# Kernel tuning notes

Measured on AMD Instinct MI355X. Metric: run time of the kernel, lower is better.

Reference implementation:

```python
import jax, jax.numpy as jnp
import numpy as np
import math

FREQ_DIM = 161
OUTPUT_DIM = 4096
RNN_DIM = 128
EMBED_DIM = 32


def conv2d(x, w, b, stride):
    # x: (B, Cin, H, W), w: (Cout, Cin, kh, kw)
    out = jax.lax.conv_general_dilated(x, w, window_strides=stride, padding='VALID',
                                       dimension_numbers=('NCHW', 'OIHW', 'NCHW'))
    return out + b[None, :, None, None]


def gru_seq(x, w_ih, w_hh, b_ih, b_hh, h0):
    # x: (B, T, D); PyTorch GRU gate order: r, z, n
    B, T, D = x.shape
    H = h0.shape[-1]
    xg = jnp.einsum('btd,gd->btg', x, w_ih) + b_ih  # (B, T, 3H)

    def step(h, xg_t):
        hg = h @ w_hh.T + b_hh
        xr, xz, xn = jnp.split(xg_t, 3, axis=-1)
        hr, hz, hn = jnp.split(hg, 3, axis=-1)
        r = jax.nn.sigmoid(xr + hr)
        z = jax.nn.sigmoid(xz + hz)
        n = jnp.tanh(xn + r * hn)
        h_new = (1 - z) * n + z * h
        return h_new, h_new

    _, hs = jax.lax.scan(step, h0, jnp.swapaxes(xg, 0, 1))
    return jnp.swapaxes(hs, 0, 1)  # (B, T, H)


def gru_cell(ix, h, w_ih, w_hh, b_ih, b_hh):
    xg = ix @ w_ih.T + b_ih
    hg = h @ w_hh.T + b_hh
    xr, xz, xn = jnp.split(xg, 3, axis=-1)
    hr, hz, hn = jnp.split(hg, 3, axis=-1)
    r = jax.nn.sigmoid(xr + hr)
    z = jax.nn.sigmoid(xz + hz)
    n = jnp.tanh(xn + r * hn)
    return (1 - z) * n + z * h


def attend(eh, dhx):
    # eh: (B, T, H), dhx: (B, H)
    scores = jnp.einsum('bth,bh->bt', eh, dhx)
    a = jax.nn.softmax(scores, axis=-1)
    return jnp.einsum('bth,bt->bh', eh, a)


def setup_inputs() -> dict:
    key = jax.random.key(0)
    ks = jax.random.split(key, 16)

    def rn(k, shape, fan_in):
        s = 1.0 / math.sqrt(fan_in)
        return jax.random.uniform(k, shape, jnp.float32, -s, s)

    B, T_audio, L = 32, 512, 128
    x = jax.random.normal(ks[0], (B, T_audio, FREQ_DIM), jnp.float32)
    y = jax.random.randint(ks[1], (B, L), 0, OUTPUT_DIM)

    conv_in = 544  # 17 * 32 after two convs on freq dim 161
    params = {
        'conv1_w': rn(ks[2], (32, 1, 5, 32), 1 * 5 * 32),
        'conv1_b': rn(ks[3], (32,), 1 * 5 * 32),
        'conv2_w': rn(ks[4], (32, 32, 5, 32), 32 * 5 * 32),
        'conv2_b': rn(ks[5], (32,), 32 * 5 * 32),
        'rnn_w_ih': rn(ks[6], (3 * RNN_DIM, conv_in), RNN_DIM),
        'rnn_w_hh': rn(ks[7], (3 * RNN_DIM, RNN_DIM), RNN_DIM),
        'rnn_b_ih': rn(ks[8], (3 * RNN_DIM,), RNN_DIM),
        'rnn_b_hh': rn(ks[9], (3 * RNN_DIM,), RNN_DIM),
        'emb': jax.random.normal(ks[10], (OUTPUT_DIM, EMBED_DIM), jnp.float32),
        'dec_w_ih': rn(ks[11], (3 * RNN_DIM, EMBED_DIM), RNN_DIM),
        'dec_w_hh': rn(ks[12], (3 * RNN_DIM, RNN_DIM), RNN_DIM),
        'dec_b_ih': rn(ks[13], (3 * RNN_DIM,), RNN_DIM),
        'dec_b_hh': rn(ks[14], (3 * RNN_DIM,), RNN_DIM),
        'fc_w': rn(ks[15], (OUTPUT_DIM, RNN_DIM), RNN_DIM),
        'fc_b': rn(jax.random.fold_in(key, 99), (OUTPUT_DIM,), RNN_DIM),
        'h_init': jnp.zeros((1, RNN_DIM), jnp.float32),
    }
    return {'x': x, 'y': y, **params}


def forward(x, y, conv1_w, conv1_b, conv2_w, conv2_b,
            rnn_w_ih, rnn_w_hh, rnn_b_ih, rnn_b_hh,
            emb, dec_w_ih, dec_w_hh, dec_b_ih, dec_b_hh,
            fc_w, fc_b, h_init):
    B = x.shape[0]
    h = x[:, None, :, :]  # (B, 1, T, F)
    h = jax.nn.relu(conv2d(h, conv1_w, conv1_b, (2, 2)))
    h = jax.nn.relu(conv2d(h, conv2_w, conv2_b, (2, 2)))  # (B, 32, t, f)
    h = jnp.transpose(h, (0, 2, 3, 1))  # (B, t, f, c)
    b, t, f, c = h.shape
    h = h.reshape(b, t, f * c)
    eh = gru_seq(h, rnn_w_ih, rnn_w_hh, rnn_b_ih, rnn_b_hh,
                 jnp.zeros((b, RNN_DIM), h.dtype))  # (B, t, 128)

    inputs = emb[y[:, :-1]]  # (B, L-1, 32)
    hx = jnp.broadcast_to(h_init, (B, RNN_DIM))
    hx = hx + attend(eh, hx)

    def step(hx, ix):
        hx = gru_cell(ix, hx, dec_w_ih, dec_w_hh, dec_b_ih, dec_b_hh)
        hx = hx + attend(eh, hx)
        return hx, hx

    _, outs = jax.lax.scan(step, hx, jnp.swapaxes(inputs, 0, 1))
    out = jnp.concatenate([hx[:, None, :], jnp.swapaxes(outs, 0, 1)], axis=1)  # (B, L, 128)
    logits = jnp.einsum('btd,od->bto', out, fc_w) + fc_b
    return logits


def reference(x, y, conv1_w, conv1_b, conv2_w, conv2_b,
              rnn_w_ih, rnn_w_hh, rnn_b_ih, rnn_b_hh,
              emb, dec_w_ih, dec_w_hh, dec_b_ih, dec_b_hh,
              fc_w, fc_b, h_init):
    return forward(x, y, conv1_w, conv1_b, conv2_w, conv2_b,
                   rnn_w_ih, rnn_w_hh, rnn_b_ih, rnn_b_hh,
                   emb, dec_w_ih, dec_w_hh, dec_b_ih, dec_b_hh,
                   fc_w, fc_b, h_init)
```

## Files before the change

kernel.cpp:

```cpp
#include <hip/hip_runtime.h>
#include <stdint.h>

typedef unsigned short u16;
typedef uint32_t u32;

typedef __bf16 bf16x8 __attribute__((ext_vector_type(8)));
typedef float f32x4 __attribute__((ext_vector_type(4)));
typedef _Float16 h2v __attribute__((ext_vector_type(2)));

union B8 { uint4 q; u32 u[4]; bf16x8 v; };

__device__ __forceinline__ u16 f2bf(float f) {
  u32 u = __float_as_uint(f);
  u32 r = (u + 0x7fffu + ((u >> 16) & 1u)) >> 16;
  return (u16)r;
}
__device__ __forceinline__ u16 f2h(float f) {
  union { _Float16 h; u16 u; } v; v.h = (_Float16)f; return v.u;
}
__device__ __forceinline__ float dot2h(u32 a, u32 b, float c) {
  union U { u32 u; h2v v; } A, B; A.u = a; B.u = b;
  return __builtin_amdgcn_fdot2(A.v, B.v, c, false);
}
__device__ __forceinline__ float sigf(float x) { return 1.f / (1.f + __expf(-x)); }
__device__ __forceinline__ float tanhf_fast(float x) {
  x = fminf(fmaxf(x, -15.f), 15.f);
  float e = __expf(2.f * x);
  return (e - 1.f) / (e + 1.f);
}

__global__ __launch_bounds__(256) void prep_k(
    const float* rnn_w_hh, const float* dec_w_hh, const float* conv1_w,
    const float* conv2_w, const float* rnn_w_ih, const float* dec_w_ih,
    const float* fc_w, const float* emb, const int* y,
    u32* wT2e, u32* wT2d, u16* w1b, u16* w2b, u16* wihb, u16* dwihb,
    u16* fcwb, u16* adec)
{
  int e = blockIdx.x * 256 + threadIdx.x;
  const int S0 = 24576, S1 = 24576, S2 = 5120, S3 = 163840, S4 = 208896,
            S5 = 12288, S6 = 524288, S7 = 130048;
  if (e < S0) { int g = e >> 6, k2 = e & 63;
    wT2e[e] = (u32)f2h(rnn_w_hh[g*128 + 2*k2]) | ((u32)f2h(rnn_w_hh[g*128 + 2*k2 + 1]) << 16);
    return; }
  e -= S0;
  if (e < S1) { int g = e >> 6, k2 = e & 63;
    wT2d[e] = (u32)f2h(dec_w_hh[g*128 + 2*k2]) | ((u32)f2h(dec_w_hh[g*128 + 2*k2 + 1]) << 16);
    return; }
  e -= S1;
  if (e < S2) { int kh = e >> 10, c = (e >> 5) & 31, kw = e & 31;
    w1b[e] = f2bf(conv1_w[c*160 + kh*32 + kw]); return; }
  e -= S2;
  if (e < S3) { int kt = e >> 10, c = (e >> 5) & 31, kw = e & 31;
    int ic = kt / 5, kh = kt - ic * 5;
    w2b[e] = f2bf(conv2_w[((c*32 + ic)*5 + kh)*32 + kw]); return; }
  e -= S3;
  if (e < S4) { wihb[e] = f2bf(rnn_w_ih[e]); return; }
  e -= S4;
  if (e < S5) { dwihb[e] = f2bf(dec_w_ih[e]); return; }
  e -= S5;
  if (e < S6) { fcwb[e] = f2bf(fc_w[e]); return; }
  e -= S6;
  if (e < S7) { int m = e >> 5, k = e & 31;
    int b = m / 127, t = m - b * 127;
    adec[e] = f2bf(emb[y[b*128 + t]*32 + k]); return; }
}

__global__ __launch_bounds__(256) void conv1_k(const float* x, const u16* w1b,
                                               const float* c1b, u16* in1b)
{
  __shared__ __align__(16) u16 slab[35 * 162];
  __shared__ __align__(16) u16 wl[5120];
  int b = blockIdx.x >> 4;
  int oh0 = (blockIdx.x & 15) * 16;
  int ih0 = oh0 * 2;
  for (int e = threadIdx.x; e < 35 * 161; e += 256) {
    int r = e / 161, iw = e - r * 161;
    int ih = ih0 + r;
    float v = (ih < 512) ? x[(b*512 + ih)*161 + iw] : 0.f;
    slab[r*162 + iw] = f2bf(v);
  }
  for (int e = threadIdx.x; e < 5120; e += 256) wl[e] = w1b[e];
  __syncthreads();
  int lane = threadIdx.x & 63, wid = threadIdx.x >> 6;
  int lrow = lane & 15, lk = (lane >> 4) * 8;
  B8 bw[5][2];
  #pragma unroll
  for (int kt = 0; kt < 5; kt++)
    #pragma unroll
    for (int ct = 0; ct < 2; ct++)
      bw[kt][ct].q = *(const uint4*)&wl[(kt*32 + ct*16 + lrow)*32 + lk];
  float bias0 = c1b[lrow], bias1 = c1b[16 + lrow];
  for (int mt = wid; mt < 65; mt += 4) {
    int m = mt * 16 + lrow;
    int ohl = m / 65, ow = m - ohl * 65;
    int ro = ohl * 324 + ow * 2 + lk;
    f32x4 a0, a1;
    #pragma unroll
    for (int i = 0; i < 4; i++) { a0[i] = 0.f; a1[i] = 0.f; }
    #pragma unroll
    for (int kt = 0; kt < 5; kt++) {
      B8 af;
      const u32* p = (const u32*)&slab[ro + kt * 162];
      af.u[0] = p[0]; af.u[1] = p[1]; af.u[2] = p[2]; af.u[3] = p[3];
      a0 = __builtin_amdgcn_mfma_f32_16x16x32_bf16(af.v, bw[kt][0].v, a0, 0, 0, 0);
      a1 = __builtin_amdgcn_mfma_f32_16x16x32_bf16(af.v, bw[kt][1].v, a1, 0, 0, 0);
    }
    int rb = mt * 16 + (lane >> 4) * 4;
    #pragma unroll
    for (int i = 0; i < 4; i++) {
      int mr = rb + i;
      int ohl2 = mr / 65, ow2 = mr - ohl2 * 65;
      int oh = oh0 + ohl2;
      if (oh < 254) {
        float v0 = fmaxf(a0[i] + bias0, 0.f);
        float v1 = fmaxf(a1[i] + bias1, 0.f);
        in1b[((b*32 + lrow)*254 + oh)*72 + ow2] = f2bf(v0);
        in1b[((b*32 + 16 + lrow)*254 + oh)*72 + ow2] = f2bf(v1);
      }
    }
  }
}

__global__ __launch_bounds__(256) void conv2_k(const u16* in1b, const u16* w2b,
                                               const float* c2b, u16* hbf)
{
  extern __shared__ char smem[];
  u16* slab = (u16*)smem;
  u16* wl = (u16*)(smem + 87552);
  int b = blockIdx.x >> 4;
  int oh0 = (blockIdx.x & 15) * 8;
  int ih0 = oh0 * 2;
  for (int q = threadIdx.x; q < 5472; q += 256) {
    int ic = q / 171;
    int rem = q - ic * 171;
    int r = rem / 9, j = rem - r * 9;
    int ih = ih0 + r;
    uint4 v = make_uint4(0u, 0u, 0u, 0u);
    if (ih < 254) v = *(const uint4*)&in1b[(((b*32 + ic)*254 + ih)*72) + j*8];
    *(uint4*)&slab[(ic*19 + r)*72 + j*8] = v;
  }
  int lane = threadIdx.x & 63, wid = threadIdx.x >> 6;
  int lrow = lane & 15, lk = (lane >> 4) * 8;
  int ohl_[3], ow_[3];
  #pragma unroll
  for (int q = 0; q < 3; q++) {
    int mt = (q == 2) ? 8 : (wid + q * 4);
    int m = mt * 16 + lrow;
    if (m > 135) m = 0;
    ohl_[q] = m / 17; ow_[q] = m - ohl_[q] * 17;
  }
  f32x4 acc[3][2];
  #pragma unroll
  for (int q = 0; q < 3; q++)
    #pragma unroll
    for (int ct = 0; ct < 2; ct++)
      #pragma unroll
      for (int i = 0; i < 4; i++) acc[q][ct][i] = 0.f;

  for (int ph = 0; ph < 5; ph++) {
    __syncthreads();
    {
      const uint4* s4 = (const uint4*)&w2b[ph * 32768];
      uint4* d4 = (uint4*)wl;
      for (int q = threadIdx.x; q < 4096; q += 256) d4[q] = s4[q];
    }
    __syncthreads();
    for (int ktl = 0; ktl < 32; ktl++) {
      int ktg = ph * 32 + ktl;
      int ic = ktg / 5, kh = ktg - ic * 5;
      B8 fb0, fb1;
      fb0.q = *(const uint4*)&wl[(ktl*32 + lrow)*32 + lk];
      fb1.q = *(const uint4*)&wl[(ktl*32 + 16 + lrow)*32 + lk];
      int base = (ic * 19 + kh) * 72 + lk;
      #pragma unroll
      for (int q = 0; q < 3; q++) {
        if (q == 2 && wid != 0) break;
        B8 af;
        const u32* p = (const u32*)&slab[base + ohl_[q] * 144 + ow_[q] * 2];
        af.u[0] = p[0]; af.u[1] = p[1]; af.u[2] = p[2]; af.u[3] = p[3];
        acc[q][0] = __builtin_amdgcn_mfma_f32_16x16x32_bf16(af.v, fb0.v, acc[q][0], 0, 0, 0);
        acc[q][1] = __builtin_amdgcn_mfma_f32_16x16x32_bf16(af.v, fb1.v, acc[q][1], 0, 0, 0);
      }
    }
  }
  #pragma unroll
  for (int q = 0; q < 3; q++) {
    if (q == 2 && wid != 0) break;
    int mt = (q == 2) ? 8 : (wid + q * 4);
    int rb = mt * 16 + (lane >> 4) * 4;
    #pragma unroll
    for (int ct = 0; ct < 2; ct++) {
      int c = ct * 16 + lrow;
      float bias = c2b[c];
      #pragma unroll
      for (int i = 0; i < 4; i++) {
        int mr = rb + i;
        if (mr < 136) {
          int ohl = mr / 17, ow = mr - ohl * 17;
          int oh = oh0 + ohl;
          if (oh < 125) {
            float v = fmaxf(acc[q][ct][i] + bias, 0.f);
            hbf[(b*125 + oh)*544 + ow*32 + c] = f2bf(v);
          }
        }
      }
    }
  }
}

__global__ __launch_bounds__(256) void gemm_k(const u16* A, const u16* Bw,
                                              const float* bias, float* C,
                                              int M, int N, int K)
{
  __shared__ __align__(16) u16 As[64 * 32];
  __shared__ __align__(16) u16 Bs[64 * 32];
  int m0 = blockIdx.x * 64, n0 = blockIdx.y * 64;
  int tid = threadIdx.x;
  int lane = tid & 63, wid = tid >> 6;
  int lrow = lane & 15, lk = (lane >> 4) * 8;
  int sr = tid >> 2, sc8 = (tid & 3) * 8;
  f32x4 acc[4];
  #pragma unroll
  for (int nt = 0; nt < 4; nt++)
    #pragma unroll
    for (int i = 0; i < 4; i++) acc[nt][i] = 0.f;
  int nkt = K >> 5;
  for (int kt = 0; kt < nkt; kt++) {
    __syncthreads();
    uint4 va = make_uint4(0u, 0u, 0u, 0u);
    int arow = m0 + sr;
    if (arow < M) va = *(const uint4*)&A[arow * K + kt * 32 + sc8];
    *(uint4*)&As[sr * 32 + sc8] = va;
    uint4 vb = *(const uint4*)&Bw[(n0 + sr) * K + kt * 32 + sc8];
    *(uint4*)&Bs[sr * 32 + sc8] = vb;
    __syncthreads();
    B8 af; af.q = *(const uint4*)&As[(wid * 16 + lrow) * 32 + lk];
    #pragma unroll
    for (int nt = 0; nt < 4; nt++) {
      B8 bb; bb.q = *(const uint4*)&Bs[(nt * 16 + lrow) * 32 + lk];
      acc[nt] = __builtin_amdgcn_mfma_f32_16x16x32_bf16(af.v, bb.v, acc[nt], 0, 0, 0);
    }
  }
  #pragma unroll
  for (int nt = 0; nt < 4; nt++) {
    int col = n0 + nt * 16 + lrow;
    float bv = bias[col];
    #pragma unroll
    for (int i = 0; i < 4; i++) {
      int row = m0 + wid * 16 + (lane >> 4) * 4 + i;
      if (row < M) C[row * N + col] = acc[nt][i] + bv;
    }
  }
}

__global__ __launch_bounds__(1024, 1) void enc_k(const u32* wT2, const float* xg,
                                                 const float* bhh_g, u16* ehk, u16* eht)
{
  __shared__ __align__(16) u32 hp[2][2][64];
  __shared__ float hg[2][1152];
  int tid = threadIdx.x;
  int g = tid >> 9, tb = tid & 511, kh = tb >> 7, t = tb & 127;
  int b = blockIdx.x * 2 + g;
  u32 w0[16], w1[16], w2[16];
  {
    const uint4* p0 = (const uint4*)(wT2 + (size_t)t * 64 + kh * 16);
    const uint4* p1 = (const uint4*)(wT2 + (size_t)(128 + t) * 64 + kh * 16);
    const uint4* p2 = (const uint4*)(wT2 + (size_t)(256 + t) * 64 + kh * 16);
    #pragma unroll
    for (int j = 0; j < 4; j++) {
      uint4 q0 = p0[j]; w0[4*j] = q0.x; w0[4*j+1] = q0.y; w0[4*j+2] = q0.z; w0[4*j+3] = q0.w;
      uint4 q1 = p1[j]; w1[4*j] = q1.x; w1[4*j+1] = q1.y; w1[4*j+2] = q1.z; w1[4*j+3] = q1.w;
      uint4 q2 = p2[j]; w2[4*j] = q2.x; w2[4*j+1] = q2.y; w2[4*j+2] = q2.z; w2[4*j+3] = q2.w;
    }
  }
  float b0 = 0.f, b1 = 0.f, b2 = 0.f, xr0 = 0.f, xr1 = 0.f, xr2 = 0.f, hreg = 0.f;
  if (kh == 0) {
    b0 = bhh_g[t]; b1 = bhh_g[128 + t]; b2 = bhh_g[256 + t];
    const float* xp = &xg[(size_t)b * 125 * 384];
    xr0 = xp[t]; xr1 = xp[128 + t]; xr2 = xp[256 + t];
    ((u16*)&hp[g][0][0])[t] = 0;
  }
  __syncthreads();
  for (int tt = 0; tt < 125; tt++) {
    const u32* hb = &hp[g][tt & 1][kh * 16];
    float r0 = 0.f, r1 = 0.f, z0 = 0.f, z1 = 0.f, n0 = 0.f, n1 = 0.f;
    #pragma unroll
    for (int j = 0; j < 4; j++) {
      uint4 hv = *(const uint4*)&hb[4*j];
      r0 = dot2h(w0[4*j+0], hv.x, r0); r1 = dot2h(w0[4*j+1], hv.y, r1);
      r0 = dot2h(w0[4*j+2], hv.z, r0); r1 = dot2h(w0[4*j+3], hv.w, r1);
      z0 = dot2h(w1[4*j+0], hv.x, z0); z1 = dot2h(w1[4*j+1], hv.y, z1);
      z0 = dot2h(w1[4*j+2], hv.z, z0); z1 = dot2h(w1[4*j+3], hv.w, z1);
      n0 = dot2h(w2[4*j+0], hv.x, n0); n1 = dot2h(w2[4*j+1], hv.y, n1);
      n0 = dot2h(w2[4*j+2], hv.z, n0); n1 = dot2h(w2[4*j+3], hv.w, n1);
    }
    if (kh) {
      float* hh = &hg[g][(kh - 1) * 384];
      hh[t] = r0 + r1; hh[128 + t] = z0 + z1; hh[256 + t] = n0 + n1;
    }
    __syncthreads();
    if (kh == 0) {
      const float* hh = &hg[g][0];
      float pr = r0 + r1 + hh[t] + hh[384 + t] + hh[768 + t];
      float pz = z0 + z1 + hh[128 + t] + hh[512 + t] + hh[896 + t];
      float pn = n0 + n1 + hh[256 + t] + hh[640 + t] + hh[1024 + t];
      float r = sigf(xr0 + pr + b0);
      float z = sigf(xr1 + pz + b1);
      float n = tanhf_fast(xr2 + r * (pn + b2));
      hreg = (1.f - z) * n + z * hreg;
      u16 hv = f2h(hreg);
      ((u16*)&hp[g][(tt & 1) ^ 1][0])[t] = hv;
      ehk[((size_t)(b*64 + (t >> 1)) * 125 + tt) * 2 + (t & 1)] = hv;
      eht[((size_t)(b*128 + t)) * 128 + tt] = hv;
      if (tt + 1 < 125) {
        const float* xq = &xg[((size_t)b * 125 + tt + 1) * 384];
        xr0 = xq[t]; xr1 = xq[128 + t]; xr2 = xq[256 + t];
      }
    }
    __syncthreads();
  }
  if (kh == 0) {
    size_t rb = ((size_t)(b*128 + t)) * 128;
    eht[rb + 125] = 0; eht[rb + 126] = 0; eht[rb + 127] = 0;
  }
}

__global__ __launch_bounds__(1024, 1) void dec_k(const u32* wT2, const u32* ehk_g,
                                                 const u32* eht_g, const float* xgd,
                                                 const float* bhh_g, const float* h_init,
                                                 u16* outb)
{
  extern __shared__ char sm[];
  int tid = threadIdx.x;
  int g = tid >> 9, tb = tid & 511, kh = tb >> 7, t = tb & 127;
  int b = blockIdx.x * 2 + g;
  char* base = sm + (size_t)g * 41024;
  u32* elK   = (u32*)base;
  float* hgP = (float*)(base + 32000);
  float* sp  = (float*)(base + 36608);
  float* ctxB= (float*)(base + 38656);
  u16* hxA   = (u16*)(base + 40192);
  u16* hxB   = (u16*)(base + 40448);
  u16* scp   = (u16*)(base + 40704);
  float* red = (float*)(base + 40960);

  u32 w0[16], w1[16], w2[16];
  {
    const uint4* p0 = (const uint4*)(wT2 + (size_t)t * 64 + kh * 16);
    const uint4* p1 = (const uint4*)(wT2 + (size_t)(128 + t) * 64 + kh * 16);
    const uint4* p2 = (const uint4*)(wT2 + (size_t)(256 + t) * 64 + kh * 16);
    #pragma unroll
    for (int j = 0; j < 4; j++) {
      uint4 q0 = p0[j]; w0[4*j] = q0.x; w0[4*j+1] = q0.y; w0[4*j+2] = q0.z; w0[4*j+3] = q0.w;
      uint4 q1 = p1[j]; w1[4*j] = q1.x; w1[4*j+1] = q1.y; w1[4*j+2] = q1.z; w1[4*j+3] = q1.w;
      uint4 q2 = p2[j]; w2[4*j] = q2.x; w2[4*j+1] = q2.y; w2[4*j+2] = q2.z; w2[4*j+3] = q2.w;
    }
  }
  u32 rowr[16];
  {
    const uint4* rp = (const uint4*)(eht_g + (size_t)b * 8192 + (size_t)t * 64 + kh * 16);
    #pragma unroll
    for (int j = 0; j < 4; j++) {
      uint4 q = rp[j]; rowr[4*j] = q.x; rowr[4*j+1] = q.y; rowr[4*j+2] = q.z; rowr[4*j+3] = q.w;
    }
  }
  for (int e = tb; e < 8000; e += 512) elK[e] = ehk_g[(size_t)b * 8000 + e];
  float b0 = 0.f, b1 = 0.f, b2 = 0.f, xr0 = 0.f, xr1 = 0.f, xr2 = 0.f;
  float hxf = 0.f, hxg = 0.f;
  if (kh == 0) {
    b0 = bhh_g[t]; b1 = bhh_g[128 + t]; b2 = bhh_g[256 + t];
    hxf = h_init[t];
    const float* xp = &xgd[(size_t)b * 127 * 384];
    xr0 = xp[t]; xr1 = xp[128 + t]; xr2 = xp[256 + t];
  }
  __syncthreads();

  for (int step = 0; step < 128; step++) {
    if (step > 0) {
      const u32* hb = (const u32*)hxB + kh * 16;
      float r0 = 0.f, r1 = 0.f, z0 = 0.f, z1 = 0.f, n0 = 0.f, n1 = 0.f;
      #pragma unroll
      for (int j = 0; j < 4; j++) {
        uint4 hv = *(const uint4*)&hb[4*j];
        r0 = dot2h(w0[4*j+0], hv.x, r0); r1 = dot2h(w0[4*j+1], hv.y, r1);
        r0 = dot2h(w0[4*j+2], hv.z, r0); r1 = dot2h(w0[4*j+3], hv.w, r1);
        z0 = dot2h(w1[4*j+0], hv.x, z0); z1 = dot2h(w1[4*j+1], hv.y, z1);
        z0 = dot2h(w1[4*j+2], hv.z, z0); z1 = dot2h(w1[4*j+3], hv.w, z1);
        n0 = dot2h(w2[4*j+0], hv.x, n0); n1 = dot2h(w2[4*j+1], hv.y, n1);
        n0 = dot2h(w2[4*j+2], hv.z, n0); n1 = dot2h(w2[4*j+3], hv.w, n1);
      }
      if (kh) {
        float* hh = &hgP[(kh - 1) * 384];
        hh[t] = r0 + r1; hh[128 + t] = z0 + z1; hh[256 + t] = n0 + n1;
      }
      __syncthreads();
      if (kh == 0) {
        float pr = r0 + r1 + hgP[t] + hgP[384 + t] + hgP[768 + t];
        float pz = z0 + z1 + hgP[128 + t] + hgP[512 + t] + hgP[896 + t];
        float pn = n0 + n1 + hgP[256 + t] + hgP[640 + t] + hgP[1024 + t];
        float r = sigf(xr0 + pr + b0);
        float z = sigf(xr1 + pz + b1);
        float n = tanhf_fast(xr2 + r * (pn + b2));
        hxg = (1.f - z) * n + z * hxf;
        ((u16*)hxA)[t] = f2h(hxg);
        if (step < 127) {
          const float* xq = &xgd[((size_t)b * 127 + step) * 384];
          xr0 = xq[t]; xr1 = xq[128 + t]; xr2 = xq[256 + t];
        }
      }
      __syncthreads();
    } else {
      if (kh == 0) { hxg = hxf; ((u16*)hxA)[t] = f2h(hxg); }
      __syncthreads();
    }
    {
      float s0 = 0.f, s1 = 0.f;
      const u32* ek = &elK[(kh * 16) * 125];
      const u32* hxA4 = (const u32*)hxA;
      #pragma unroll
      for (int j = 0; j < 4; j++) {
        uint4 aw = *(const uint4*)&hxA4[kh * 16 + 4*j];
        s0 = dot2h(ek[(4*j+0)*125 + t], aw.x, s0);
        s1 = dot2h(ek[(4*j+1)*125 + t], aw.y, s1);
        s0 = dot2h(ek[(4*j+2)*125 + t], aw.z, s0);
        s1 = dot2h(ek[(4*j+3)*125 + t], aw.w, s1);
      }
      sp[kh * 128 + t] = s0 + s1;
    }
    __syncthreads();
    if (kh == 0) {
      float s = (t < 125) ? (sp[t] + sp[128 + t] + sp[256 + t] + sp[384 + t]) : -1e30f;
      float mw = s;
      #pragma unroll
      for (int o = 32; o > 0; o >>= 1) mw = fmaxf(mw, __shfl_xor(mw, o));
      float ev = (t < 125) ? __expf(s - mw) : 0.f;
      float sw = ev;
      #pragma unroll
      for (int o = 32; o > 0; o >>= 1) sw += __shfl_xor(sw, o);
      ((u16*)scp)[t] = f2h(ev);
      if ((t & 63) == 0) { int wv = t >> 6; red[wv*2] = mw; red[wv*2 + 1] = sw; }
    }
    __syncthreads();
    float m0r = red[0], S0r = red[1], m1r = red[2], S1r = red[3];
    float M = fmaxf(m0r, m1r);
    float f0 = __expf(m0r - M), f1 = __expf(m1r - M);
    float inv = 1.f / (f0 * S0r + f1 * S1r);
    float c0 = 0.f, c1 = 0.f;
    {
      const u32* scp4 = (const u32*)scp;
      #pragma unroll
      for (int j = 0; j < 4; j++) {
        uint4 sw4 = *(const uint4*)&scp4[kh * 16 + 4*j];
        c0 = dot2h(rowr[4*j+0], sw4.x, c0); c1 = dot2h(rowr[4*j+1], sw4.y, c1);
        c0 = dot2h(rowr[4*j+2], sw4.z, c0); c1 = dot2h(rowr[4*j+3], sw4.w, c1);
      }
    }
    if (kh) ctxB[(kh - 1) * 128 + t] = c0 + c1;
    __syncthreads();
    if (kh == 0) {
      float ctx = ((c0 + c1) + ctxB[t]) * f0 + (ctxB[128 + t] + ctxB[256 + t]) * f1;
      hxf = hxg + ctx * inv;
      outb[((size_t)(b * 128) + step) * 128 + t] = f2bf(hxf);
      ((u16*)hxB)[t] = f2h(hxf);
    }
    __syncthreads();
  }
}

extern "C" void kernel_launch(void* const* d_in, const int* in_sizes, int n_in,
                              void* d_out, int out_size, void* d_ws, size_t ws_size,
                              hipStream_t stream)
{
  const float* x        = (const float*)d_in[0];
  const int*   y        = (const int*)d_in[1];
  const float* conv1_w  = (const float*)d_in[2];
  const float* conv1_b  = (const float*)d_in[3];
  const float* conv2_w  = (const float*)d_in[4];
  const float* conv2_b  = (const float*)d_in[5];
  const float* rnn_w_ih = (const float*)d_in[6];
  const float* rnn_w_hh = (const float*)d_in[7];
  const float* rnn_b_ih = (const float*)d_in[8];
  const float* rnn_b_hh = (const float*)d_in[9];
  const float* emb      = (const float*)d_in[10];
  const float* dec_w_ih = (const float*)d_in[11];
  const float* dec_w_hh = (const float*)d_in[12];
  const float* dec_b_ih = (const float*)d_in[13];
  const float* dec_b_hh = (const float*)d_in[14];
  const float* fc_w     = (const float*)d_in[15];
  const float* fc_b     = (const float*)d_in[16];
  const float* h_init   = (const float*)d_in[17];
  float* logits = (float*)d_out;

  char* ws = (char*)d_ws;
  size_t off = 0;
  auto alloc = [&](size_t bytes) { char* p = ws + off; off = (off + bytes + 255) & ~(size_t)255; return p; };
  u16* in1b  = (u16*)alloc(37453824);
  u16* hbf   = (u16*)alloc(4352000);
  float* xge = (float*)alloc(6144000);
  u32* ehb_k = (u32*)alloc(1024000);
  u32* ehb_t = (u32*)alloc(1048576);
  float* xgd = (float*)alloc(6242304);
  u16* adec  = (u16*)alloc(260096);
  u16* outb  = (u16*)alloc(1048576);
  u32* wT2e  = (u32*)alloc(98304);
  u32* wT2d  = (u32*)alloc(98304);
  u16* w1b   = (u16*)alloc(10240);
  u16* w2b   = (u16*)alloc(327680);
  u16* wihb  = (u16*)alloc(417792);
  u16* dwihb = (u16*)alloc(24576);
  u16* fcwb  = (u16*)alloc(1048576);

  hipFuncSetAttribute((const void*)conv2_k, hipFuncAttributeMaxDynamicSharedMemorySize, 153088);
  hipFuncSetAttribute((const void*)dec_k,   hipFuncAttributeMaxDynamicSharedMemorySize, 82048);

  prep_k<<<4272, 256, 0, stream>>>(rnn_w_hh, dec_w_hh, conv1_w, conv2_w, rnn_w_ih,
                                   dec_w_ih, fc_w, emb, y,
                                   wT2e, wT2d, w1b, w2b, wihb, dwihb, fcwb, adec);
  conv1_k<<<512, 256, 0, stream>>>(x, w1b, conv1_b, in1b);
  conv2_k<<<512, 256, 153088, stream>>>(in1b, w2b, conv2_b, hbf);
  gemm_k<<<dim3(63, 6), 256, 0, stream>>>(hbf, wihb, rnn_b_ih, xge, 4000, 384, 544);
  gemm_k<<<dim3(64, 6), 256, 0, stream>>>(adec, dwihb, dec_b_ih, xgd, 4064, 384, 32);
  enc_k<<<16, 1024, 0, stream>>>(wT2e, xge, rnn_b_hh, (u16*)ehb_k, (u16*)ehb_t);
  dec_k<<<16, 1024, 82048, stream>>>(wT2d, ehb_k, ehb_t, xgd, dec_b_hh, h_init, outb);
  gemm_k<<<dim3(64, 64), 256, 0, stream>>>(outb, fcwb, fc_b, logits, 4096, 4096, 128);
}
```

Before: 604.0 us.

## Reduce K-split partials with wave shuffles instead of LDS and barriers

Remaps threads so the four K-slices of each hidden unit sit in the same wavefront (16 units by 4 slices per wave). The GRU gate partial sums, attention scores and context partials are then combined with xor-shuffles rather than written to shared memory and read back after a block barrier. This removes several __syncthreads per recurrent step in both the encoder and decoder, and shrinks the decoder's shared memory. Softmax statistics now come from 8 per-wave partials combined in every thread, and the encoded-state copy into LDS uses 16-byte loads. The risk is extra shuffle and exp work per step, plus a different LDS access pattern from the new thread mapping.

Result: slower. 707.3 us (+17.1%).

```diff
diff --git a/kernel.cpp b/kernel.cpp
--- a/kernel.cpp
+++ b/kernel.cpp
@@ -257,9 +257,10 @@
                                                  const float* bhh_g, u16* ehk, u16* eht)
 {
   __shared__ __align__(16) u32 hp[2][2][64];
-  __shared__ float hg[2][1152];
   int tid = threadIdx.x;
-  int g = tid >> 9, tb = tid & 511, kh = tb >> 7, t = tb & 127;
+  int g = tid >> 9, tb = tid & 511;
+  int wb = tb >> 6, l = tb & 63, kh = l >> 4, tl = l & 15;
+  int t = wb * 16 + tl;
   int b = blockIdx.x * 2 + g;
   u32 w0[16], w1[16], w2[16];
   {
@@ -294,16 +295,11 @@
       n0 = dot2h(w2[4*j+0], hv.x, n0); n1 = dot2h(w2[4*j+1], hv.y, n1);
       n0 = dot2h(w2[4*j+2], hv.z, n0); n1 = dot2h(w2[4*j+3], hv.w, n1);
     }
-    if (kh) {
-      float* hh = &hg[g][(kh - 1) * 384];
-      hh[t] = r0 + r1; hh[128 + t] = z0 + z1; hh[256 + t] = n0 + n1;
-    }
-    __syncthreads();
+    float pr = r0 + r1, pz = z0 + z1, pn = n0 + n1;
+    pr += __shfl_xor(pr, 16); pr += __shfl_xor(pr, 32);
+    pz += __shfl_xor(pz, 16); pz += __shfl_xor(pz, 32);
+    pn += __shfl_xor(pn, 16); pn += __shfl_xor(pn, 32);
     if (kh == 0) {
-      const float* hh = &hg[g][0];
-      float pr = r0 + r1 + hh[t] + hh[384 + t] + hh[768 + t];
-      float pz = z0 + z1 + hh[128 + t] + hh[512 + t] + hh[896 + t];
-      float pn = n0 + n1 + hh[256 + t] + hh[640 + t] + hh[1024 + t];
       float r = sigf(xr0 + pr + b0);
       float z = sigf(xr1 + pz + b1);
       float n = tanhf_fast(xr2 + r * (pn + b2));
@@ -332,17 +328,16 @@
 {
   extern __shared__ char sm[];
   int tid = threadIdx.x;
-  int g = tid >> 9, tb = tid & 511, kh = tb >> 7, t = tb & 127;
-  int b = blockIdx.x * 2 + g;
-  char* base = sm + (size_t)g * 41024;
-  u32* elK   = (u32*)base;
-  float* hgP = (float*)(base + 32000);
-  float* sp  = (float*)(base + 36608);
-  float* ctxB= (float*)(base + 38656);
-  u16* hxA   = (u16*)(base + 40192);
-  u16* hxB   = (u16*)(base + 40448);
-  u16* scp   = (u16*)(base + 40704);
-  float* red = (float*)(base + 40960);
+  int g = tid >> 9, tb = tid & 511;
+  int wb = tb >> 6, l = tb & 63, kh = l >> 4, tl = l & 15;
+  int t = wb * 16 + tl;
+  int bg = blockIdx.x * 2 + g;
+  char* base = sm + (size_t)g * 33024;
+  u32* elK = (u32*)base;
+  u16* hxA = (u16*)(base + 32000);
+  u16* hxB = (u16*)(base + 32256);
+  u16* scp = (u16*)(base + 32512);
+  float* red = (float*)(base + 32768);
 
   u32 w0[16], w1[16], w2[16];
   {
@@ -358,19 +353,23 @@
   }
   u32 rowr[16];
   {
-    const uint4* rp = (const uint4*)(eht_g + (size_t)b * 8192 + (size_t)t * 64 + kh * 16);
+    const uint4* rp = (const uint4*)(eht_g + (size_t)bg * 8192 + (size_t)t * 64 + kh * 16);
     #pragma unroll
     for (int j = 0; j < 4; j++) {
       uint4 q = rp[j]; rowr[4*j] = q.x; rowr[4*j+1] = q.y; rowr[4*j+2] = q.z; rowr[4*j+3] = q.w;
     }
   }
-  for (int e = tb; e < 8000; e += 512) elK[e] = ehk_g[(size_t)b * 8000 + e];
+  {
+    const uint4* s4 = (const uint4*)(ehk_g + (size_t)bg * 8000);
+    uint4* d4 = (uint4*)elK;
+    for (int q = tb; q < 2000; q += 512) d4[q] = s4[q];
+  }
   float b0 = 0.f, b1 = 0.f, b2 = 0.f, xr0 = 0.f, xr1 = 0.f, xr2 = 0.f;
   float hxf = 0.f, hxg = 0.f;
   if (kh == 0) {
     b0 = bhh_g[t]; b1 = bhh_g[128 + t]; b2 = bhh_g[256 + t];
     hxf = h_init[t];
-    const float* xp = &xgd[(size_t)b * 127 * 384];
+    const float* xp = &xgd[(size_t)bg * 127 * 384];
     xr0 = xp[t]; xr1 = xp[128 + t]; xr2 = xp[256 + t];
   }
   __syncthreads();
@@ -389,34 +388,29 @@
         n0 = dot2h(w2[4*j+0], hv.x, n0); n1 = dot2h(w2[4*j+1], hv.y, n1);
         n0 = dot2h(w2[4*j+2], hv.z, n0); n1 = dot2h(w2[4*j+3], hv.w, n1);
       }
-      if (kh) {
-        float* hh = &hgP[(kh - 1) * 384];
-        hh[t] = r0 + r1; hh[128 + t] = z0 + z1; hh[256 + t] = n0 + n1;
-      }
-      __syncthreads();
+      float pr = r0 + r1, pz = z0 + z1, pn = n0 + n1;
+      pr += __shfl_xor(pr, 16); pr += __shfl_xor(pr, 32);
+      pz += __shfl_xor(pz, 16); pz += __shfl_xor(pz, 32);
+      pn += __shfl_xor(pn, 16); pn += __shfl_xor(pn, 32);
       if (kh == 0) {
-        float pr = r0 + r1 + hgP[t] + hgP[384 + t] + hgP[768 + t];
-        float pz = z0 + z1 + hgP[128 + t] + hgP[512 + t] + hgP[896 + t];
-        float pn = n0 + n1 + hgP[256 + t] + hgP[640 + t] + hgP[1024 + t];
         float r = sigf(xr0 + pr + b0);
         float z = sigf(xr1 + pz + b1);
         float n = tanhf_fast(xr2 + r * (pn + b2));
         hxg = (1.f - z) * n + z * hxf;
-        ((u16*)hxA)[t] = f2h(hxg);
+        hxA[t] = f2h(hxg);
         if (step < 127) {
-          const float* xq = &xgd[((size_t)b * 127 + step) * 384];
+          const float* xq = &xgd[((size_t)bg * 127 + step) * 384];
           xr0 = xq[t]; xr1 = xq[128 + t]; xr2 = xq[256 + t];
         }
       }
-      __syncthreads();
     } else {
-      if (kh == 0) { hxg = hxf; ((u16*)hxA)[t] = f2h(hxg); }
-      __syncthreads();
-    }
+      if (kh == 0) { hxg = hxf; hxA[t] = f2h(hxg); }
+    }
+    __syncthreads();
     {
+      const u32* ek = elK + (kh * 16) * 125;
+      const u32* hxA4 = (const u32*)hxA;
       float s0 = 0.f, s1 = 0.f;
-      const u32* ek = &elK[(kh * 16) * 125];
-      const u32* hxA4 = (const u32*)hxA;
       #pragma unroll
       for (int j = 0; j < 4; j++) {
         uint4 aw = *(const uint4*)&hxA4[kh * 16 + 4*j];
@@ -425,43 +419,63 @@
         s0 = dot2h(ek[(4*j+2)*125 + t], aw.z, s0);
         s1 = dot2h(ek[(4*j+3)*125 + t], aw.w, s1);
       }
-      sp[kh * 128 + t] = s0 + s1;
-    }
-    __syncthreads();
-    if (kh == 0) {
-      float s = (t < 125) ? (sp[t] + sp[128 + t] + sp[256 + t] + sp[384 + t]) : -1e30f;
+      float s = s0 + s1;
+      s += __shfl_xor(s, 16); s += __shfl_xor(s, 32);
+      if (t >= 125) s = -1e30f;
       float mw = s;
-      #pragma unroll
-      for (int o = 32; o > 0; o >>= 1) mw = fmaxf(mw, __shfl_xor(mw, o));
+      mw = fmaxf(mw, __shfl_xor(mw, 1));
+      mw = fmaxf(mw, __shfl_xor(mw, 2));
+      mw = fmaxf(mw, __shfl_xor(mw, 4));
+      mw = fmaxf(mw, __shfl_xor(mw, 8));
       float ev = (t < 125) ? __expf(s - mw) : 0.f;
       float sw = ev;
-      #pragma unroll
-      for (int o = 32; o > 0; o >>= 1) sw += __shfl_xor(sw, o);
-      ((u16*)scp)[t] = f2h(ev);
-      if ((t & 63) == 0) { int wv = t >> 6; red[wv*2] = mw; red[wv*2 + 1] = sw; }
-    }
-    __syncthreads();
-    float m0r = red[0], S0r = red[1], m1r = red[2], S1r = red[3];
-    float M = fmaxf(m0r, m1r);
-    float f0 = __expf(m0r - M), f1 = __expf(m1r - M);
-    float inv = 1.f / (f0 * S0r + f1 * S1r);
-    float c0 = 0.f, c1 = 0.f;
+      sw += __shfl_xor(sw, 1);
+      sw += __shfl_xor(sw, 2);
+      sw += __shfl_xor(sw, 4);
+      sw += __shfl_xor(sw, 8);
+      if (kh == 0) scp[t] = f2h(ev);
+      if (l == 0) { red[wb * 2] = mw; red[wb * 2 + 1] = sw; }
+    }
+    __syncthreads();
     {
+      float4 ra = *(const float4*)&red[0];
+      float4 rb = *(const float4*)&red[4];
+      float4 rc = *(const float4*)&red[8];
+      float4 rd = *(const float4*)&red[12];
+      float M = fmaxf(fmaxf(fmaxf(ra.x, ra.z), fmaxf(rb.x, rb.z)),
+                      fmaxf(fmaxf(rc.x, rc.z), fmaxf(rd.x, rd.z)));
+      float f0 = __expf(ra.x - M), f1 = __expf(ra.z - M);
+      float f2 = __expf(rb.x - M), f3 = __expf(rb.z - M);
+      float f4 = __expf(rc.x - M), f5 = __expf(rc.z - M);
+      float f6 = __expf(rd.x - M), f7 = __expf(rd.z - M);
+      float inv = 1.f / (f0*ra.y + f1*ra.w + f2*rb.y + f3*rb.w +
+                         f4*rc.y + f5*rc.w + f6*rd.y + f7*rd.w);
+      float fa, fb;
+      if (kh == 0)      { fa = f0; fb = f1; }
+      else if (kh == 1) { fa = f2; fb = f3; }
+      else if (kh == 2) { fa = f4; fb = f5; }
+      else              { fa = f6; fb = f7; }
       const u32* scp4 = (const u32*)scp;
-      #pragma unroll
-      for (int j = 0; j < 4; j++) {
-        uint4 sw4 = *(const uint4*)&scp4[kh * 16 + 4*j];
-        c0 = dot2h(rowr[4*j+0], sw4.x, c0); c1 = dot2h(rowr[4*j+1], sw4.y, c1);
-        c0 = dot2h(rowr[4*j+2], sw4.z, c0); c1 = dot2h(rowr[4*j+3], sw4.w, c1);
-      }
-    }
-    if (kh) ctxB[(kh - 1) * 128 + t] = c0 + c1;
-    __syncthreads();
-    if (kh == 0) {
-      float ctx = ((c0 + c1) + ctxB[t]) * f0 + (ctxB[128 + t] + ctxB[256 + t]) * f1;
-      hxf = hxg + ctx * inv;
-      outb[((size_t)(b * 128) + step) * 128 + t] = f2bf(hxf);
-      ((u16*)hxB)[t] = f2h(hxf);
+      uint4 sA = *(const uint4*)&scp4[kh * 16];
+      uint4 sB = *(const uint4*)&scp4[kh * 16 + 4];
+      uint4 sC = *(const uint4*)&scp4[kh * 16 + 8];
+      uint4 sD = *(const uint4*)&scp4[kh * 16 + 12];
+      float ca = 0.f, cb = 0.f;
+      ca = dot2h(rowr[0], sA.x, ca); ca = dot2h(rowr[1], sA.y, ca);
+      ca = dot2h(rowr[2], sA.z, ca); ca = dot2h(rowr[3], sA.w, ca);
+      ca = dot2h(rowr[4], sB.x, ca); ca = dot2h(rowr[5], sB.y, ca);
+      ca = dot2h(rowr[6], sB.z, ca); ca = dot2h(rowr[7], sB.w, ca);
+      cb = dot2h(rowr[8], sC.x, cb); cb = dot2h(rowr[9], sC.y, cb);
+      cb = dot2h(rowr[10], sC.z, cb); cb = dot2h(rowr[11], sC.w, cb);
+      cb = dot2h(rowr[12], sD.x, cb); cb = dot2h(rowr[13], sD.y, cb);
+      cb = dot2h(rowr[14], sD.z, cb); cb = dot2h(rowr[15], sD.w, cb);
+      float part = ca * fa + cb * fb;
+      part += __shfl_xor(part, 16); part += __shfl_xor(part, 32);
+      if (kh == 0) {
+        hxf = hxg + part * inv;
+        outb[((size_t)(bg * 128) + step) * 128 + t] = f2bf(hxf);
+        hxB[t] = f2h(hxf);
+      }
     }
     __syncthreads();
   }
@@ -511,7 +525,7 @@
   u16* fcwb  = (u16*)alloc(1048576);
 
   hipFuncSetAttribute((const void*)conv2_k, hipFuncAttributeMaxDynamicSharedMemorySize, 153088);
-  hipFuncSetAttribute((const void*)dec_k,   hipFuncAttributeMaxDynamicSharedMemorySize, 82048);
+  hipFuncSetAttribute((const void*)dec_k,   hipFuncAttributeMaxDynamicSharedMemorySize, 66048);
 
   prep_k<<<4272, 256, 0, stream>>>(rnn_w_hh, dec_w_hh, conv1_w, conv2_w, rnn_w_ih,
                                    dec_w_ih, fc_w, emb, y,
@@ -521,6 +535,6 @@
   gemm_k<<<dim3(63, 6), 256, 0, stream>>>(hbf, wihb, rnn_b_ih, xge, 4000, 384, 544);
   gemm_k<<<dim3(64, 6), 256, 0, stream>>>(adec, dwihb, dec_b_ih, xgd, 4064, 384, 32);
   enc_k<<<16, 1024, 0, stream>>>(wT2e, xge, rnn_b_hh, (u16*)ehb_k, (u16*)ehb_t);
-  dec_k<<<16, 1024, 82048, stream>>>(wT2d, ehb_k, ehb_t, xgd, dec_b_hh, h_init, outb);
+  dec_k<<<16, 1024, 66048, stream>>>(wT2d, ehb_k, ehb_t, xgd, dec_b_hh, h_init, outb);
   gemm_k<<<dim3(64, 64), 256, 0, stream>>>(outb, fcwb, fc_b, logits, 4096, 4096, 128);
 }
```
